# Optimization experiments

Measured on AMD Instinct MI355X. Metric: run time of the kernel, lower is better.

The kernel has to match this reference:

```python
import jax, jax.numpy as jnp
import numpy as np

N = 100000      # nodes
E = 1600000     # edges (avg degree 16)
DIN, DH, DOUT = 128, 64, 32


def setup_inputs() -> dict:
    key = jax.random.key(0)
    ks = jax.random.split(key, 6)
    x = jax.random.normal(ks[0], (N, DIN), dtype=jnp.float32)
    edge_index = jax.random.randint(ks[1], (2, E), 0, N, dtype=jnp.int32)
    # GCNConv weights (glorot-ish scale), biases zero-init as in PyG default
    W1 = jax.random.normal(ks[2], (DIN, DH), dtype=jnp.float32) / np.sqrt(DIN).astype(np.float32)
    b1 = jnp.zeros((DH,), dtype=jnp.float32)
    W2 = jax.random.normal(ks[3], (DH, DOUT), dtype=jnp.float32) / np.sqrt(DH).astype(np.float32)
    b2 = jnp.zeros((DOUT,), dtype=jnp.float32)
    # fc is hard-reset in reset_parameters: weight=ones, bias=zeros
    fc_w = jnp.ones((1, DOUT), dtype=jnp.float32)
    fc_b = jnp.zeros((1,), dtype=jnp.float32)
    return {"x": x, "edge_index": edge_index, "W1": W1, "b1": b1,
            "W2": W2, "b2": b2, "fc_w": fc_w, "fc_b": fc_b}


def gcn_conv(x, W, b, src, dst, n):
    """PyG GCNConv: add self-loops, symmetric deg normalization, x@W then aggregate."""
    h = x @ W                                             # [n, dout] transform first
    ones = jnp.ones(src.shape[0], dtype=x.dtype)
    deg = jax.ops.segment_sum(ones, dst, num_segments=n) + 1.0   # +1 for self-loop
    dinv = jax.lax.rsqrt(deg)
    coef = dinv[src] * dinv[dst]                          # [E] edge norm
    agg = jax.ops.segment_sum(h[src] * coef[:, None], dst, num_segments=n)
    agg = agg + h * (1.0 / deg)[:, None]                  # self-loop term: dinv_i*dinv_i
    return agg + b


def reference(x, edge_index, W1, b1, W2, b2, fc_w, fc_b):
    src, dst = edge_index[0], edge_index[1]
    h = jax.nn.relu(gcn_conv(x, W1, b1, src, dst, N))
    h = jax.nn.relu(gcn_conv(h, W2, b2, src, dst, N))
    scores = (h @ fc_w.T + fc_b)[:, 0]                    # Linear(out,1) then squeeze
    return scores, h
```

## Files before the change

kernel.cpp:

```cpp
#include <hip/hip_runtime.h>

#define NN 100000
#define EE 1600000
#define DIN 128
#define DH 64
#define DOUT 32

#define BSH 8
#define BNODES 256
#define NBUCK ((NN + BNODES - 1) / BNODES)
#define BCAP 4608
#define CHUNK 4096
#define NCHUNK ((EE + CHUNK - 1) / CHUNK)
#define GEMMB ((NN + 127) / 128)

typedef unsigned short ush;
typedef __attribute__((ext_vector_type(8))) short bf16x8;
typedef __attribute__((ext_vector_type(4))) float f32x4;
typedef __attribute__((ext_vector_type(2))) float f32x2;

__device__ __forceinline__ float bflo(unsigned u) {
    union { unsigned u; float f; } c; c.u = u << 16; return c.f;
}
__device__ __forceinline__ float bfhi(unsigned u) {
    union { unsigned u; float f; } c; c.u = u & 0xffff0000u; return c.f;
}
__device__ __forceinline__ ush f2bf(float f) {
    union { float f; unsigned u; } c; c.f = f;
    unsigned r = c.u + 0x7fff + ((c.u >> 16) & 1);
    return (ush)(r >> 16);
}

__device__ __forceinline__ void pka(f32x2& a, f32x2 b) {
    asm("v_pk_add_f32 %0, %0, %1" : "+v"(a) : "v"(b));
}
__device__ __forceinline__ void pkfma(f32x2& d, f32x2 a, f32x2 b) {
    asm("v_pk_fma_f32 %0, %1, %2, %0" : "+v"(d) : "v"(a), "v"(b));
}
__device__ __forceinline__ void pkmul(f32x2& a, f32x2 b) {
    asm("v_pk_mul_f32 %0, %0, %1" : "+v"(a) : "v"(b));
}
__device__ __forceinline__ f32x2 up2(unsigned u) {
    f32x2 p; p.x = bflo(u); p.y = bfhi(u); return p;
}

__global__ void init_kernel(int* __restrict__ gdeg, int* __restrict__ bcur) {
    int i = blockIdx.x * 256 + threadIdx.x;
    if (i < NN) gdeg[i] = 0;
    if (i < NBUCK) bcur[i] = i * BCAP;
}

__global__ __launch_bounds__(256) void binA_kernel(const int* __restrict__ src,
                                                   const int* __restrict__ dst,
                                                   int* __restrict__ bcur,
                                                   int* __restrict__ gdeg,
                                                   unsigned* __restrict__ tmp) {
    __shared__ int hist[NBUCK];
    __shared__ int scn[NBUCK];
    __shared__ int cur[NBUCK];
    __shared__ int gb[NBUCK];
    __shared__ int s2[256];
    __shared__ unsigned staged[CHUNK];
    __shared__ int gaddr[CHUNK];
    int t = threadIdx.x;
    for (int i = t; i < NBUCK; i += 256) hist[i] = 0;
    __syncthreads();
    int e0 = blockIdx.x * CHUNK;
    int nE = min(CHUNK, EE - e0);

    int my_e[16], my_bk[16];
#pragma unroll
    for (int k = 0; k < 16; k++) {
        int li = t + k * 256;
        bool ok = li < nE;
        int idx = ok ? (e0 + li) : e0;
        int d = dst[idx];
        int s = src[idx];
        int b = d >> BSH;
        my_e[k] = (s << 8) | (d & 255);
        my_bk[k] = ok ? b : -1;
        if (ok) {
            atomicAdd(&hist[b], 1);
            atomicAdd(&gdeg[d], 1);
        }
    }
    __syncthreads();
    int a0 = (2 * t < NBUCK) ? hist[2 * t] : 0;
    int a1 = (2 * t + 1 < NBUCK) ? hist[2 * t + 1] : 0;
    s2[t] = a0 + a1;
    __syncthreads();
    for (int off = 1; off < 256; off <<= 1) {
        int x = (t >= off) ? s2[t - off] : 0;
        __syncthreads();
        s2[t] += x;
        __syncthreads();
    }
    int excl = s2[t] - a0 - a1;
    if (2 * t < NBUCK)     { scn[2 * t] = excl;          cur[2 * t] = excl; }
    if (2 * t + 1 < NBUCK) { scn[2 * t + 1] = excl + a0; cur[2 * t + 1] = excl + a0; }
    __syncthreads();
    for (int i = t; i < NBUCK; i += 256) {
        int h = hist[i];
        if (h) gb[i] = atomicAdd(&bcur[i], h) - scn[i];
    }
    __syncthreads();
#pragma unroll
    for (int k = 0; k < 16; k++) {
        int b = my_bk[k];
        if (b >= 0) {
            int lp = atomicAdd(&cur[b], 1);
            staged[lp] = (unsigned)my_e[k];
            gaddr[lp] = gb[b] + lp;
        }
    }
    __syncthreads();
    for (int i = t; i < nE; i += 256)
        tmp[gaddr[i]] = staged[i];
}

__global__ __launch_bounds__(256) void fatBG_kernel(const unsigned* __restrict__ tmp,
                                                    const int* __restrict__ bcur,
                                                    const int* __restrict__ gdeg,
                                                    const float* __restrict__ x,
                                                    const float* __restrict__ W1,
                                                    int* __restrict__ csr,
                                                    int* __restrict__ offs,
                                                    int* __restrict__ ends,
                                                    float* __restrict__ dinv,
                                                    ush* __restrict__ Hs1) {
    __shared__ int cur[BNODES], sc[BNODES];
    constexpr int KP = DIN + 8;
    __shared__ __align__(16) ush Wt[DH * KP];
    const int t = threadIdx.x;

    if (blockIdx.x < NBUCK) {
        int b = blockIdx.x;
        int e0 = b * BCAP, e1 = bcur[b];
        int node = (b << BSH) + t;
        int v = (node < NN) ? gdeg[node] : 0;
        sc[t] = v;
        __syncthreads();
        for (int off = 1; off < 256; off <<= 1) {
            int xv = (t >= off) ? sc[t - off] : 0;
            __syncthreads();
            sc[t] += xv;
            __syncthreads();
        }
        int excl = sc[t] - v;
        cur[t] = e0 + excl;
        if (node < NN) {
            offs[node] = e0 + excl;
            ends[node] = e0 + excl + v;
            dinv[node] = 1.0f / sqrtf((float)v + 1.0f);
        }
        __syncthreads();
        for (int i = e0 + t; i < e1; i += 256) {
            unsigned u = tmp[i];
            int pos = atomicAdd(&cur[u & 255], 1);
            csr[pos] = (int)(u >> 8);
        }
        return;
    }

    const int row0 = (blockIdx.x - NBUCK) * 128;
    constexpr int NCT = DH / 16;
    for (int i = t; i < DIN * (DH / 4); i += 256) {
        int k = i / (DH / 4), n4 = i % (DH / 4);
        float4 v = *(const float4*)&W1[k * DH + n4 * 4];
        Wt[(n4 * 4 + 0) * KP + k] = f2bf(v.x);
        Wt[(n4 * 4 + 1) * KP + k] = f2bf(v.y);
        Wt[(n4 * 4 + 2) * KP + k] = f2bf(v.z);
        Wt[(n4 * 4 + 3) * KP + k] = f2bf(v.w);
    }
    __syncthreads();

    const int wave = t >> 6, lane = t & 63;
    const int m = lane & 15, quad = lane >> 4;
    const int wrow = wave * 32;

    f32x4 acc[2][NCT];
#pragma unroll
    for (int rt = 0; rt < 2; rt++)
#pragma unroll
        for (int ct = 0; ct < NCT; ct++) acc[rt][ct] = (f32x4){0.f, 0.f, 0.f, 0.f};

#pragma unroll
    for (int kc = 0; kc < DIN / 32; kc++) {
        int koff = kc * 32 + quad * 8;
        bf16x8 bfr[NCT];
#pragma unroll
        for (int ct = 0; ct < NCT; ct++)
            bfr[ct] = *(const bf16x8*)&Wt[(ct * 16 + m) * KP + koff];
#pragma unroll
        for (int rt = 0; rt < 2; rt++) {
            int row = row0 + wrow + rt * 16 + m;
            float4 va = make_float4(0.f, 0.f, 0.f, 0.f), vb = va;
            if (row < NN) {
                va = *(const float4*)&x[(size_t)row * DIN + koff];
                vb = *(const float4*)&x[(size_t)row * DIN + koff + 4];
            }
            union { bf16x8 v; ush s[8]; } A;
            A.s[0] = f2bf(va.x); A.s[1] = f2bf(va.y); A.s[2] = f2bf(va.z); A.s[3] = f2bf(va.w);
            A.s[4] = f2bf(vb.x); A.s[5] = f2bf(vb.y); A.s[6] = f2bf(vb.z); A.s[7] = f2bf(vb.w);
#pragma unroll
            for (int ct = 0; ct < NCT; ct++)
                acc[rt][ct] = __builtin_amdgcn_mfma_f32_16x16x32_bf16(A.v, bfr[ct], acc[rt][ct], 0, 0, 0);
        }
    }
#pragma unroll
    for (int rt = 0; rt < 2; rt++) {
#pragma unroll
        for (int reg = 0; reg < 4; reg++) {
            int row = row0 + wrow + rt * 16 + quad * 4 + reg;
            if (row < NN) {
                float s = 1.0f / sqrtf((float)gdeg[row] + 1.0f);
#pragma unroll
                for (int ct = 0; ct < NCT; ct++)
                    Hs1[(size_t)row * DH + ct * 16 + m] = f2bf(acc[rt][ct][reg] * s);
            }
        }
    }
}

#define ACCP(u4) { pka(ac0, up2(u4.x)); pka(ac1, up2(u4.y)); \
                   pka(ac2, up2(u4.z)); pka(ac3, up2(u4.w)); }

#define ZINV(u4, v) { u4.x = (v) ? u4.x : 0u; u4.y = (v) ? u4.y : 0u; \
                      u4.z = (v) ? u4.z : 0u; u4.w = (v) ? u4.w : 0u; }

#define BFLY(msk) { f32x2 t_;                                           \
    t_.x = __shfl_xor(ac0.x, msk); t_.y = __shfl_xor(ac0.y, msk); pka(ac0, t_); \
    t_.x = __shfl_xor(ac1.x, msk); t_.y = __shfl_xor(ac1.y, msk); pka(ac1, t_); \
    t_.x = __shfl_xor(ac2.x, msk); t_.y = __shfl_xor(ac2.y, msk); pka(ac2, t_); \
    t_.x = __shfl_xor(ac3.x, msk); t_.y = __shfl_xor(ac3.y, msk); pka(ac3, t_); }

__global__ __launch_bounds__(256) void gather1_fused_kernel(const int* __restrict__ offs,
                                                            const int* __restrict__ ends,
                                                            const float* __restrict__ dinv,
                                                            const ush* __restrict__ Hs,
                                                            const int* __restrict__ csr,
                                                            const float* __restrict__ b1,
                                                            const float* __restrict__ W2,
                                                            ush* __restrict__ Hs2) {
    __shared__ __align__(16) float Wp[32 * 68];
    {
        int t = threadIdx.x;
        int lp = t >> 3, r = t & 7;
        int srow = (lp & 7) * 8 + r, scol = (lp >> 3) * 8;
        float4 va = *(const float4*)&W2[srow * DOUT + scol];
        float4 vb = *(const float4*)&W2[srow * DOUT + scol + 4];
        *(float4*)&Wp[lp * 68 + r * 8] = va;
        *(float4*)&Wp[lp * 68 + r * 8 + 4] = vb;
    }
    __syncthreads();

    int wid = (blockIdx.x * 256 + threadIdx.x) >> 6;
    int lane = threadIdx.x & 63;
    int node = wid * 2 + (lane >> 5);
    if (node >= NN) return;
    int l = lane & 31;
    int es = l >> 3;
    int fg = l & 7;
    int start = offs[node], end = ends[node];
    float dv = dinv[node];
    uint4 su = *(const uint4*)&Hs[node * DH + fg * 8];
    f32x2 ac0 = {0.f, 0.f}, ac1 = {0.f, 0.f}, ac2 = {0.f, 0.f}, ac3 = {0.f, 0.f};

    int base = start + es;
    {
        int p0 = base, p1 = base + 4, p2 = base + 8,
            p3 = base + 12, p4 = base + 16, p5 = base + 20;
        bool v0 = p0 < end, v1 = p1 < end, v2 = p2 < end,
             v3 = p3 < end, v4 = p4 < end, v5 = p5 < end;
        int s0 = csr[v0 ? p0 : 0], s1 = csr[v1 ? p1 : 0], s2 = csr[v2 ? p2 : 0],
            s3 = csr[v3 ? p3 : 0], s4 = csr[v4 ? p4 : 0], s5 = csr[v5 ? p5 : 0];
        uint4 u0 = *(const uint4*)&Hs[s0 * DH + fg * 8];
        uint4 u1 = *(const uint4*)&Hs[s1 * DH + fg * 8];
        uint4 u2 = *(const uint4*)&Hs[s2 * DH + fg * 8];
        uint4 u3 = *(const uint4*)&Hs[s3 * DH + fg * 8];
        uint4 u4 = *(const uint4*)&Hs[s4 * DH + fg * 8];
        uint4 u5 = *(const uint4*)&Hs[s5 * DH + fg * 8];
        ZINV(u0, v0) ZINV(u1, v1) ZINV(u2, v2)
        ZINV(u3, v3) ZINV(u4, v4) ZINV(u5, v5)
        ACCP(u0) ACCP(u1) ACCP(u2) ACCP(u3) ACCP(u4) ACCP(u5)
    }
    for (int k = base + 24; k < end; k += 4) {
        int s = csr[k];
        uint4 u = *(const uint4*)&Hs[s * DH + fg * 8];
        ACCP(u)
    }
    BFLY(8) BFLY(16)

    float4 ba = *(const float4*)&b1[fg * 8];
    float4 bb = *(const float4*)&b1[fg * 8 + 4];
    f32x2 dvp; dvp.x = dv; dvp.y = dv;
    pka(ac0, up2(su.x)); pka(ac1, up2(su.y)); pka(ac2, up2(su.z)); pka(ac3, up2(su.w));
    f32x2 h0; h0.x = ba.x; h0.y = ba.y;
    f32x2 h1; h1.x = ba.z; h1.y = ba.w;
    f32x2 h2; h2.x = bb.x; h2.y = bb.y;
    f32x2 h3; h3.x = bb.z; h3.y = bb.w;
    pkfma(h0, dvp, ac0); pkfma(h1, dvp, ac1); pkfma(h2, dvp, ac2); pkfma(h3, dvp, ac3);
    h0.x = fmaxf(h0.x, 0.f); h0.y = fmaxf(h0.y, 0.f);
    h1.x = fmaxf(h1.x, 0.f); h1.y = fmaxf(h1.y, 0.f);
    h2.x = fmaxf(h2.x, 0.f); h2.y = fmaxf(h2.y, 0.f);
    h3.x = fmaxf(h3.x, 0.f); h3.y = fmaxf(h3.y, 0.f);

    const float* wl = &Wp[l * 68];
    float hs_[8] = {h0.x, h0.y, h1.x, h1.y, h2.x, h2.y, h3.x, h3.y};
    f32x2 p0 = {0.f, 0.f}, p1 = {0.f, 0.f}, p2 = {0.f, 0.f}, p3 = {0.f, 0.f};
#pragma unroll
    for (int r = 0; r < 8; r++) {
        float4 wa = *(const float4*)&wl[r * 8];
        float4 wb = *(const float4*)&wl[r * 8 + 4];
        f32x2 hr; hr.x = hs_[r]; hr.y = hs_[r];
        f32x2 w01; w01.x = wa.x; w01.y = wa.y;
        f32x2 w23; w23.x = wa.z; w23.y = wa.w;
        f32x2 w45; w45.x = wb.x; w45.y = wb.y;
        f32x2 w67; w67.x = wb.z; w67.y = wb.w;
        pkfma(p0, hr, w01); pkfma(p1, hr, w23);
        pkfma(p2, hr, w45); pkfma(p3, hr, w67);
    }
#pragma unroll
    for (int msk = 1; msk <= 4; msk <<= 1) {
        f32x2 t_;
        t_.x = __shfl_xor(p0.x, msk); t_.y = __shfl_xor(p0.y, msk); pka(p0, t_);
        t_.x = __shfl_xor(p1.x, msk); t_.y = __shfl_xor(p1.y, msk); pka(p1, t_);
        t_.x = __shfl_xor(p2.x, msk); t_.y = __shfl_xor(p2.y, msk); pka(p2, t_);
        t_.x = __shfl_xor(p3.x, msk); t_.y = __shfl_xor(p3.y, msk); pka(p3, t_);
    }
    if (fg == 0) {
        pkmul(p0, dvp); pkmul(p1, dvp); pkmul(p2, dvp); pkmul(p3, dvp);
        ushort4 oa, ob;
        oa.x = f2bf(p0.x); oa.y = f2bf(p0.y); oa.z = f2bf(p1.x); oa.w = f2bf(p1.y);
        ob.x = f2bf(p2.x); ob.y = f2bf(p2.y); ob.z = f2bf(p3.x); ob.w = f2bf(p3.y);
        *(ushort4*)&Hs2[node * DOUT + es * 8] = oa;
        *(ushort4*)&Hs2[node * DOUT + es * 8 + 4] = ob;
    }
}

__global__ __launch_bounds__(256) void gather2_kernel(const int* __restrict__ offs,
                                                      const int* __restrict__ ends,
                                                      const float* __restrict__ dinv,
                                                      const ush* __restrict__ Hs,
                                                      const int* __restrict__ csr,
                                                      const float* __restrict__ b2,
                                                      const float* __restrict__ fcw,
                                                      const float* __restrict__ fcb,
                                                      float* __restrict__ h2,
                                                      float* __restrict__ scores) {
    int wid = (blockIdx.x * 256 + threadIdx.x) >> 6;
    int lane = threadIdx.x & 63;
    int node = wid * 2 + (lane >> 5);
    if (node >= NN) return;
    int l = lane & 31;
    int es = l >> 2;
    int fg = l & 3;
    int start = offs[node], end = ends[node];
    float dv = dinv[node];
    uint4 su = *(const uint4*)&Hs[node * DOUT + fg * 8];
    f32x2 ac0 = {0.f, 0.f}, ac1 = {0.f, 0.f}, ac2 = {0.f, 0.f}, ac3 = {0.f, 0.f};

    int base = start + es;
    {
        int p0 = base, p1 = base + 8, p2 = base + 16, p3 = base + 24;
        bool v0 = p0 < end, v1 = p1 < end, v2 = p2 < end, v3 = p3 < end;
        int s0 = csr[v0 ? p0 : 0], s1 = csr[v1 ? p1 : 0],
            s2 = csr[v2 ? p2 : 0], s3 = csr[v3 ? p3 : 0];
        uint4 u0 = *(const uint4*)&Hs[s0 * DOUT + fg * 8];
        uint4 u1 = *(const uint4*)&Hs[s1 * DOUT + fg * 8];
        uint4 u2 = *(const uint4*)&Hs[s2 * DOUT + fg * 8];
        uint4 u3 = *(const uint4*)&Hs[s3 * DOUT + fg * 8];
        ZINV(u0, v0) ZINV(u1, v1) ZINV(u2, v2) ZINV(u3, v3)
        ACCP(u0) ACCP(u1) ACCP(u2) ACCP(u3)
    }
    for (int k = base + 32; k < end; k += 8) {
        int s = csr[k];
        uint4 u = *(const uint4*)&Hs[s * DOUT + fg * 8];
        ACCP(u)
    }
    BFLY(4) BFLY(8) BFLY(16)

    float4 ba = *(const float4*)&b2[fg * 8];
    float4 bb = *(const float4*)&b2[fg * 8 + 4];
    f32x2 dvp; dvp.x = dv; dvp.y = dv;
    pka(ac0, up2(su.x)); pka(ac1, up2(su.y)); pka(ac2, up2(su.z)); pka(ac3, up2(su.w));
    f32x2 h0; h0.x = ba.x; h0.y = ba.y;
    f32x2 h1; h1.x = ba.z; h1.y = ba.w;
    f32x2 h2v; h2v.x = bb.x; h2v.y = bb.y;
    f32x2 h3; h3.x = bb.z; h3.y = bb.w;
    pkfma(h0, dvp, ac0); pkfma(h1, dvp, ac1); pkfma(h2v, dvp, ac2); pkfma(h3, dvp, ac3);
    h0.x = fmaxf(h0.x, 0.f); h0.y = fmaxf(h0.y, 0.f);
    h1.x = fmaxf(h1.x, 0.f); h1.y = fmaxf(h1.y, 0.f);
    h2v.x = fmaxf(h2v.x, 0.f); h2v.y = fmaxf(h2v.y, 0.f);
    h3.x = fmaxf(h3.x, 0.f); h3.y = fmaxf(h3.y, 0.f);
    if (es == 0) {
        float4 o0, o1;
        o0.x = h0.x; o0.y = h0.y; o0.z = h1.x; o0.w = h1.y;
        o1.x = h2v.x; o1.y = h2v.y; o1.z = h3.x; o1.w = h3.y;
        *(float4*)&h2[node * DOUT + fg * 8] = o0;
        *(float4*)&h2[node * DOUT + fg * 8 + 4] = o1;
    }
    float4 fa = *(const float4*)&fcw[fg * 8];
    float4 fb = *(const float4*)&fcw[fg * 8 + 4];
    f32x2 dp = {0.f, 0.f};
    f32x2 f01; f01.x = fa.x; f01.y = fa.y;
    f32x2 f23; f23.x = fa.z; f23.y = fa.w;
    f32x2 f45; f45.x = fb.x; f45.y = fb.y;
    f32x2 f67; f67.x = fb.z; f67.y = fb.w;
    pkfma(dp, h0, f01); pkfma(dp, h1, f23); pkfma(dp, h2v, f45); pkfma(dp, h3, f67);
    float sv = dp.x + dp.y;
    sv += __shfl_xor(sv, 1); sv += __shfl_xor(sv, 2);
    if (l == 0) scores[node] = sv + fcb[0];
}

extern "C" void kernel_launch(void* const* d_in, const int* in_sizes, int n_in,
                              void* d_out, int out_size, void* d_ws, size_t ws_size,
                              hipStream_t stream) {
    const float* x   = (const float*)d_in[0];
    const int*   ei  = (const int*)d_in[1];
    const float* W1  = (const float*)d_in[2];
    const float* b1  = (const float*)d_in[3];
    const float* W2  = (const float*)d_in[4];
    const float* b2  = (const float*)d_in[5];
    const float* fcw = (const float*)d_in[6];
    const float* fcb = (const float*)d_in[7];
    const int* src = ei;
    const int* dst = ei + EE;

    float* ws = (float*)d_ws;
    float* dinv    = ws;
    int*   offs    = (int*)(ws + 100352);
    int*   ends    = (int*)(ws + 200704);
    int*   bcur    = (int*)(ws + 301056);
    int*   csr     = (int*)(ws + 301568);
    unsigned* tmp  = (unsigned*)(ws + 2103296);
    ush*   Hs1     = (ush*)(ws + 3905024);
    ush*   Hs2     = (ush*)(ws + 7105024);
    int*   gdeg    = (int*)(ws + 8705024);

    float* out    = (float*)d_out;
    float* scores = out;
    float* h2     = out + NN;

    const int T = 256;
    init_kernel<<<(NN + 255) / 256, T, 0, stream>>>(gdeg, bcur);
    binA_kernel<<<NCHUNK, T, 0, stream>>>(src, dst, bcur, gdeg, tmp);
    fatBG_kernel<<<NBUCK + GEMMB, T, 0, stream>>>(tmp, bcur, gdeg, x, W1,
                                                  csr, offs, ends, dinv, Hs1);
    gather1_fused_kernel<<<(NN / 2 * 64 + T - 1) / T, T, 0, stream>>>(offs, ends, dinv, Hs1, csr, b1, W2, Hs2);
    gather2_kernel<<<(NN / 2 * 64 + T - 1) / T, T, 0, stream>>>(offs, ends, dinv, Hs2, csr, b2, fcw, fcb, h2, scores);
}
```

Before: 264.4 us.

## Overlap edge binning with layer-1 GEMM and drop global degree atomics

The edge-binning pass is merged into the same launch as the x@W1 GEMM, so the two independent stages run concurrently in one kernel, with a shared-memory union to cap LDS use. Per-node degrees are no longer built with global atomics. Instead, each bucket block counts them from its binned edges in shared memory. The GEMM therefore writes unscaled H, and the first gather multiplies each neighbor row by dinv[src], which adds one extra scalar load per edge. The binning chunk size is halved to 2048 so the merged kernel fits its LDS budget, and the init kernel now only resets the bucket cursors.

```diff
diff --git a/kernel.cpp b/kernel.cpp
--- a/kernel.cpp
+++ b/kernel.cpp
@@ -10,7 +10,7 @@
 #define BNODES 256
 #define NBUCK ((NN + BNODES - 1) / BNODES)
 #define BCAP 4608
-#define CHUNK 4096
+#define CHUNK 2048
 #define NCHUNK ((EE + CHUNK - 1) / CHUNK)
 #define GEMMB ((NN + 127) / 128)
 
@@ -44,133 +44,97 @@
     f32x2 p; p.x = bflo(u); p.y = bfhi(u); return p;
 }
 
-__global__ void init_kernel(int* __restrict__ gdeg, int* __restrict__ bcur) {
+__global__ void init_bcur_kernel(int* __restrict__ bcur) {
     int i = blockIdx.x * 256 + threadIdx.x;
-    if (i < NN) gdeg[i] = 0;
     if (i < NBUCK) bcur[i] = i * BCAP;
 }
 
-__global__ __launch_bounds__(256) void binA_kernel(const int* __restrict__ src,
-                                                   const int* __restrict__ dst,
-                                                   int* __restrict__ bcur,
-                                                   int* __restrict__ gdeg,
-                                                   unsigned* __restrict__ tmp) {
-    __shared__ int hist[NBUCK];
-    __shared__ int scn[NBUCK];
-    __shared__ int cur[NBUCK];
-    __shared__ int gb[NBUCK];
-    __shared__ int s2[256];
-    __shared__ unsigned staged[CHUNK];
-    __shared__ int gaddr[CHUNK];
-    int t = threadIdx.x;
-    for (int i = t; i < NBUCK; i += 256) hist[i] = 0;
-    __syncthreads();
-    int e0 = blockIdx.x * CHUNK;
-    int nE = min(CHUNK, EE - e0);
-
-    int my_e[16], my_bk[16];
-#pragma unroll
-    for (int k = 0; k < 16; k++) {
-        int li = t + k * 256;
-        bool ok = li < nE;
-        int idx = ok ? (e0 + li) : e0;
-        int d = dst[idx];
-        int s = src[idx];
-        int b = d >> BSH;
-        my_e[k] = (s << 8) | (d & 255);
-        my_bk[k] = ok ? b : -1;
-        if (ok) {
-            atomicAdd(&hist[b], 1);
-            atomicAdd(&gdeg[d], 1);
-        }
-    }
-    __syncthreads();
-    int a0 = (2 * t < NBUCK) ? hist[2 * t] : 0;
-    int a1 = (2 * t + 1 < NBUCK) ? hist[2 * t + 1] : 0;
-    s2[t] = a0 + a1;
-    __syncthreads();
-    for (int off = 1; off < 256; off <<= 1) {
-        int x = (t >= off) ? s2[t - off] : 0;
-        __syncthreads();
-        s2[t] += x;
-        __syncthreads();
-    }
-    int excl = s2[t] - a0 - a1;
-    if (2 * t < NBUCK)     { scn[2 * t] = excl;          cur[2 * t] = excl; }
-    if (2 * t + 1 < NBUCK) { scn[2 * t + 1] = excl + a0; cur[2 * t + 1] = excl + a0; }
-    __syncthreads();
-    for (int i = t; i < NBUCK; i += 256) {
-        int h = hist[i];
-        if (h) gb[i] = atomicAdd(&bcur[i], h) - scn[i];
-    }
-    __syncthreads();
-#pragma unroll
-    for (int k = 0; k < 16; k++) {
-        int b = my_bk[k];
-        if (b >= 0) {
-            int lp = atomicAdd(&cur[b], 1);
-            staged[lp] = (unsigned)my_e[k];
-            gaddr[lp] = gb[b] + lp;
-        }
-    }
-    __syncthreads();
-    for (int i = t; i < nE; i += 256)
-        tmp[gaddr[i]] = staged[i];
-}
-
-__global__ __launch_bounds__(256) void fatBG_kernel(const unsigned* __restrict__ tmp,
-                                                    const int* __restrict__ bcur,
-                                                    const int* __restrict__ gdeg,
+union __align__(16) FatLDS {
+    struct {
+        int hist[NBUCK], scn[NBUCK], cur[NBUCK], gb[NBUCK];
+        int s2[256];
+        unsigned staged[CHUNK];
+        int gaddr[CHUNK];
+    } a;
+    struct {
+        ush wt[DH * (DIN + 8)];
+    } g;
+};
+
+__global__ __launch_bounds__(256) void fatAG_kernel(const int* __restrict__ src,
+                                                    const int* __restrict__ dst,
+                                                    int* __restrict__ bcur,
+                                                    unsigned* __restrict__ tmp,
                                                     const float* __restrict__ x,
                                                     const float* __restrict__ W1,
-                                                    int* __restrict__ csr,
-                                                    int* __restrict__ offs,
-                                                    int* __restrict__ ends,
-                                                    float* __restrict__ dinv,
                                                     ush* __restrict__ Hs1) {
-    __shared__ int cur[BNODES], sc[BNODES];
+    __shared__ FatLDS L;
+    const int t = threadIdx.x;
+
+    if (blockIdx.x < NCHUNK) {
+        for (int i = t; i < NBUCK; i += 256) L.a.hist[i] = 0;
+        __syncthreads();
+        int e0 = blockIdx.x * CHUNK;
+        int nE = min(CHUNK, EE - e0);
+
+        int my_e[8], my_bk[8];
+#pragma unroll
+        for (int k = 0; k < 8; k++) {
+            int li = t + k * 256;
+            bool ok = li < nE;
+            int idx = ok ? (e0 + li) : e0;
+            int d = dst[idx];
+            int s = src[idx];
+            int b = d >> BSH;
+            my_e[k] = (s << 8) | (d & 255);
+            my_bk[k] = ok ? b : -1;
+            if (ok) atomicAdd(&L.a.hist[b], 1);
+        }
+        __syncthreads();
+        int a0 = (2 * t < NBUCK) ? L.a.hist[2 * t] : 0;
+        int a1 = (2 * t + 1 < NBUCK) ? L.a.hist[2 * t + 1] : 0;
+        L.a.s2[t] = a0 + a1;
+        __syncthreads();
+        for (int off = 1; off < 256; off <<= 1) {
+            int xv = (t >= off) ? L.a.s2[t - off] : 0;
+            __syncthreads();
+            L.a.s2[t] += xv;
+            __syncthreads();
+        }
+        int excl = L.a.s2[t] - a0 - a1;
+        if (2 * t < NBUCK)     { L.a.scn[2 * t] = excl;          L.a.cur[2 * t] = excl; }
+        if (2 * t + 1 < NBUCK) { L.a.scn[2 * t + 1] = excl + a0; L.a.cur[2 * t + 1] = excl + a0; }
+        __syncthreads();
+        for (int i = t; i < NBUCK; i += 256) {
+            int h = L.a.hist[i];
+            if (h) L.a.gb[i] = atomicAdd(&bcur[i], h) - L.a.scn[i];
+        }
+        __syncthreads();
+#pragma unroll
+        for (int k = 0; k < 8; k++) {
+            int b = my_bk[k];
+            if (b >= 0) {
+                int lp = atomicAdd(&L.a.cur[b], 1);
+                L.a.staged[lp] = (unsigned)my_e[k];
+                L.a.gaddr[lp] = L.a.gb[b] + lp;
+            }
+        }
+        __syncthreads();
+        for (int i = t; i < nE; i += 256)
+            tmp[L.a.gaddr[i]] = L.a.staged[i];
+        return;
+    }
+
     constexpr int KP = DIN + 8;
-    __shared__ __align__(16) ush Wt[DH * KP];
-    const int t = threadIdx.x;
-
-    if (blockIdx.x < NBUCK) {
-        int b = blockIdx.x;
-        int e0 = b * BCAP, e1 = bcur[b];
-        int node = (b << BSH) + t;
-        int v = (node < NN) ? gdeg[node] : 0;
-        sc[t] = v;
-        __syncthreads();
-        for (int off = 1; off < 256; off <<= 1) {
-            int xv = (t >= off) ? sc[t - off] : 0;
-            __syncthreads();
-            sc[t] += xv;
-            __syncthreads();
-        }
-        int excl = sc[t] - v;
-        cur[t] = e0 + excl;
-        if (node < NN) {
-            offs[node] = e0 + excl;
-            ends[node] = e0 + excl + v;
-            dinv[node] = 1.0f / sqrtf((float)v + 1.0f);
-        }
-        __syncthreads();
-        for (int i = e0 + t; i < e1; i += 256) {
-            unsigned u = tmp[i];
-            int pos = atomicAdd(&cur[u & 255], 1);
-            csr[pos] = (int)(u >> 8);
-        }
-        return;
-    }
-
-    const int row0 = (blockIdx.x - NBUCK) * 128;
     constexpr int NCT = DH / 16;
+    const int row0 = (blockIdx.x - NCHUNK) * 128;
     for (int i = t; i < DIN * (DH / 4); i += 256) {
         int k = i / (DH / 4), n4 = i % (DH / 4);
         float4 v = *(const float4*)&W1[k * DH + n4 * 4];
-        Wt[(n4 * 4 + 0) * KP + k] = f2bf(v.x);
-        Wt[(n4 * 4 + 1) * KP + k] = f2bf(v.y);
-        Wt[(n4 * 4 + 2) * KP + k] = f2bf(v.z);
-        Wt[(n4 * 4 + 3) * KP + k] = f2bf(v.w);
+        L.g.wt[(n4 * 4 + 0) * KP + k] = f2bf(v.x);
+        L.g.wt[(n4 * 4 + 1) * KP + k] = f2bf(v.y);
+        L.g.wt[(n4 * 4 + 2) * KP + k] = f2bf(v.z);
+        L.g.wt[(n4 * 4 + 3) * KP + k] = f2bf(v.w);
     }
     __syncthreads();
 
@@ -190,7 +154,7 @@
         bf16x8 bfr[NCT];
 #pragma unroll
         for (int ct = 0; ct < NCT; ct++)
-            bfr[ct] = *(const bf16x8*)&Wt[(ct * 16 + m) * KP + koff];
+            bfr[ct] = *(const bf16x8*)&L.g.wt[(ct * 16 + m) * KP + koff];
 #pragma unroll
         for (int rt = 0; rt < 2; rt++) {
             int row = row0 + wrow + rt * 16 + m;
@@ -213,17 +177,57 @@
         for (int reg = 0; reg < 4; reg++) {
             int row = row0 + wrow + rt * 16 + quad * 4 + reg;
             if (row < NN) {
-                float s = 1.0f / sqrtf((float)gdeg[row] + 1.0f);
 #pragma unroll
                 for (int ct = 0; ct < NCT; ct++)
-                    Hs1[(size_t)row * DH + ct * 16 + m] = f2bf(acc[rt][ct][reg] * s);
+                    Hs1[(size_t)row * DH + ct * 16 + m] = f2bf(acc[rt][ct][reg]);
             }
         }
+    }
+}
+
+__global__ __launch_bounds__(256) void binB_kernel(const unsigned* __restrict__ tmp,
+                                                   const int* __restrict__ bcur,
+                                                   int* __restrict__ csr,
+                                                   int* __restrict__ offs,
+                                                   int* __restrict__ ends,
+                                                   float* __restrict__ dinv) {
+    __shared__ int hist[BNODES], cur[BNODES], sc[BNODES];
+    int b = blockIdx.x, t = threadIdx.x;
+    int e0 = b * BCAP, e1 = bcur[b];
+    hist[t] = 0;
+    __syncthreads();
+    for (int i = e0 + t; i < e1; i += 256) atomicAdd(&hist[tmp[i] & 255], 1);
+    __syncthreads();
+    int v = hist[t];
+    sc[t] = v;
+    __syncthreads();
+    for (int off = 1; off < 256; off <<= 1) {
+        int x = (t >= off) ? sc[t - off] : 0;
+        __syncthreads();
+        sc[t] += x;
+        __syncthreads();
+    }
+    int excl = sc[t] - v;
+    cur[t] = e0 + excl;
+    int node = (b << BSH) + t;
+    if (node < NN) {
+        offs[node] = e0 + excl;
+        ends[node] = e0 + excl + v;
+        dinv[node] = 1.0f / sqrtf((float)v + 1.0f);
+    }
+    __syncthreads();
+    for (int i = e0 + t; i < e1; i += 256) {
+        unsigned u = tmp[i];
+        int pos = atomicAdd(&cur[u & 255], 1);
+        csr[pos] = (int)(u >> 8);
     }
 }
 
 #define ACCP(u4) { pka(ac0, up2(u4.x)); pka(ac1, up2(u4.y)); \
                    pka(ac2, up2(u4.z)); pka(ac3, up2(u4.w)); }
+
+#define ACCW(u4, dd) { pkfma(ac0, dd, up2(u4.x)); pkfma(ac1, dd, up2(u4.y)); \
+                       pkfma(ac2, dd, up2(u4.z)); pkfma(ac3, dd, up2(u4.w)); }
 
 #define ZINV(u4, v) { u4.x = (v) ? u4.x : 0u; u4.y = (v) ? u4.y : 0u; \
                       u4.z = (v) ? u4.z : 0u; u4.w = (v) ? u4.w : 0u; }
@@ -274,27 +278,37 @@
              v3 = p3 < end, v4 = p4 < end, v5 = p5 < end;
         int s0 = csr[v0 ? p0 : 0], s1 = csr[v1 ? p1 : 0], s2 = csr[v2 ? p2 : 0],
             s3 = csr[v3 ? p3 : 0], s4 = csr[v4 ? p4 : 0], s5 = csr[v5 ? p5 : 0];
+        float d0 = v0 ? dinv[s0] : 0.f, d1 = v1 ? dinv[s1] : 0.f,
+              d2 = v2 ? dinv[s2] : 0.f, d3 = v3 ? dinv[s3] : 0.f,
+              d4 = v4 ? dinv[s4] : 0.f, d5 = v5 ? dinv[s5] : 0.f;
         uint4 u0 = *(const uint4*)&Hs[s0 * DH + fg * 8];
         uint4 u1 = *(const uint4*)&Hs[s1 * DH + fg * 8];
         uint4 u2 = *(const uint4*)&Hs[s2 * DH + fg * 8];
         uint4 u3 = *(const uint4*)&Hs[s3 * DH + fg * 8];
         uint4 u4 = *(const uint4*)&Hs[s4 * DH + fg * 8];
         uint4 u5 = *(const uint4*)&Hs[s5 * DH + fg * 8];
-        ZINV(u0, v0) ZINV(u1, v1) ZINV(u2, v2)
-        ZINV(u3, v3) ZINV(u4, v4) ZINV(u5, v5)
-        ACCP(u0) ACCP(u1) ACCP(u2) ACCP(u3) ACCP(u4) ACCP(u5)
+        f32x2 dd;
+        dd.x = d0; dd.y = d0; ACCW(u0, dd)
+        dd.x = d1; dd.y = d1; ACCW(u1, dd)
+        dd.x = d2; dd.y = d2; ACCW(u2, dd)
+        dd.x = d3; dd.y = d3; ACCW(u3, dd)
+        dd.x = d4; dd.y = d4; ACCW(u4, dd)
+        dd.x = d5; dd.y = d5; ACCW(u5, dd)
     }
     for (int k = base + 24; k < end; k += 4) {
         int s = csr[k];
+        float d = dinv[s];
         uint4 u = *(const uint4*)&Hs[s * DH + fg * 8];
-        ACCP(u)
+        f32x2 dd; dd.x = d; dd.y = d;
+        ACCW(u, dd)
     }
     BFLY(8) BFLY(16)
 
     float4 ba = *(const float4*)&b1[fg * 8];
     float4 bb = *(const float4*)&b1[fg * 8 + 4];
     f32x2 dvp; dvp.x = dv; dvp.y = dv;
-    pka(ac0, up2(su.x)); pka(ac1, up2(su.y)); pka(ac2, up2(su.z)); pka(ac3, up2(su.w));
+    pkfma(ac0, dvp, up2(su.x)); pkfma(ac1, dvp, up2(su.y));
+    pkfma(ac2, dvp, up2(su.z)); pkfma(ac3, dvp, up2(su.w));
     f32x2 h0; h0.x = ba.x; h0.y = ba.y;
     f32x2 h1; h1.x = ba.z; h1.y = ba.w;
     f32x2 h2; h2.x = bb.x; h2.y = bb.y;
@@ -436,17 +450,15 @@
     unsigned* tmp  = (unsigned*)(ws + 2103296);
     ush*   Hs1     = (ush*)(ws + 3905024);
     ush*   Hs2     = (ush*)(ws + 7105024);
-    int*   gdeg    = (int*)(ws + 8705024);
 
     float* out    = (float*)d_out;
     float* scores = out;
     float* h2     = out + NN;
 
     const int T = 256;
-    init_kernel<<<(NN + 255) / 256, T, 0, stream>>>(gdeg, bcur);
-    binA_kernel<<<NCHUNK, T, 0, stream>>>(src, dst, bcur, gdeg, tmp);
-    fatBG_kernel<<<NBUCK + GEMMB, T, 0, stream>>>(tmp, bcur, gdeg, x, W1,
-                                                  csr, offs, ends, dinv, Hs1);
+    init_bcur_kernel<<<2, 256, 0, stream>>>(bcur);
+    fatAG_kernel<<<NCHUNK + GEMMB, T, 0, stream>>>(src, dst, bcur, tmp, x, W1, Hs1);
+    binB_kernel<<<NBUCK, T, 0, stream>>>(tmp, bcur, csr, offs, ends, dinv);
     gather1_fused_kernel<<<(NN / 2 * 64 + T - 1) / T, T, 0, stream>>>(offs, ends, dinv, Hs1, csr, b1, W2, Hs2);
     gather2_kernel<<<(NN / 2 * 64 + T - 1) / T, T, 0, stream>>>(offs, ends, dinv, Hs2, csr, b2, fcw, fcb, h2, scores);
 }
```

Result: faster. 222.8 us (-15.7%).
